# Kernel tuning notes

Hardware: AMD Instinct MI355X
Metric: run time of the kernel (lower is better)

## Reference

```python
import jax, jax.numpy as jnp
import numpy as np

KH, KW = 3, 3
STRIDE = (1, 1)
PAD = (1, 1)
DIL = (1, 1)
DG = 1  # num_deformable_groups


def _out_size(h, pad, dil, k, stride):
    return (h + 2 * pad - (dil * (k - 1) + 1)) // stride + 1


def setup_inputs() -> dict:
    key = jax.random.key(0)
    k1, k2, k3 = jax.random.split(key, 3)
    B, Cin, H, W = 8, 128, 64, 64
    Cout = 128
    Ho = _out_size(H, PAD[0], DIL[0], KH, STRIDE[0])
    Wo = _out_size(W, PAD[1], DIL[1], KW, STRIDE[1])
    x = jax.random.normal(k1, (B, Cin, H, W), jnp.float32)
    offset = jax.random.normal(k2, (B, 2 * DG * KH * KW, Ho, Wo), jnp.float32)
    n = Cin * KH * KW
    stdv = 1.0 / np.sqrt(n)
    weight = jax.random.uniform(k3, (Cout, Cin, KH, KW), jnp.float32, -stdv, stdv)
    return {"x": x, "offset": offset, "weight": weight}


def deform_conv2d(x, offset, weight):
    B, Cin, H, W = x.shape
    Cout, _, kh, kw = weight.shape
    K = kh * kw
    Ho = _out_size(H, PAD[0], DIL[0], kh, STRIDE[0])
    Wo = _out_size(W, PAD[1], DIL[1], kw, STRIDE[1])
    G = DG
    Cg = Cin // G

    # base sampling grid per kernel tap: [kh,kw,Ho,Wo]
    by = (jnp.arange(kh) * DIL[0])[:, None, None, None] + (jnp.arange(Ho) * STRIDE[0] - PAD[0])[None, None, :, None]
    bx = (jnp.arange(kw) * DIL[1])[None, :, None, None] + (jnp.arange(Wo) * STRIDE[1] - PAD[1])[None, None, None, :]
    by = jnp.broadcast_to(by, (kh, kw, Ho, Wo)).reshape(K, Ho, Wo).astype(x.dtype)
    bx = jnp.broadcast_to(bx, (kh, kw, Ho, Wo)).reshape(K, Ho, Wo).astype(x.dtype)

    # offset layout: channel = g*2*K + 2*k + {0: dy, 1: dx}
    off = offset.reshape(B, G, K, 2, Ho, Wo)
    py = by[None, None] + off[:, :, :, 0]  # [B,G,K,Ho,Wo]
    px = bx[None, None] + off[:, :, :, 1]

    y0 = jnp.floor(py).astype(jnp.int32)
    x0 = jnp.floor(px).astype(jnp.int32)
    wy = (py - y0).reshape(B, G, 1, -1)  # fractional parts, [B,G,1,K*Ho*Wo]
    wx = (px - x0).reshape(B, G, 1, -1)

    xg = x.reshape(B, G, Cg, H * W)
    N = K * Ho * Wo

    def gather(yi, xi):
        valid = ((yi >= 0) & (yi < H) & (xi >= 0) & (xi < W)).reshape(B, G, 1, N)
        idx = (jnp.clip(yi, 0, H - 1) * W + jnp.clip(xi, 0, W - 1)).reshape(B, G, 1, N)
        v = jnp.take_along_axis(xg, jnp.broadcast_to(idx, (B, G, Cg, N)), axis=3)
        return v * valid.astype(x.dtype)

    v00 = gather(y0, x0)
    v01 = gather(y0, x0 + 1)
    v10 = gather(y0 + 1, x0)
    v11 = gather(y0 + 1, x0 + 1)

    cols = (v00 * (1 - wy) * (1 - wx) + v01 * (1 - wy) * wx
            + v10 * wy * (1 - wx) + v11 * wy * wx)
    cols = cols.reshape(B, G, Cg, K, Ho, Wo)  # deformable im2col columns

    wr = weight.reshape(Cout, G, Cg, K)
    return jnp.einsum('ogck,bgcknm->bonm', wr, cols)


def reference(x, offset, weight):
    return deform_conv2d(x, offset, weight)
```

## Files before the change

### kernel.cpp

```cpp
#include <hip/hip_runtime.h>
#include <hip/hip_bf16.h>

typedef __attribute__((ext_vector_type(4))) float f32x4;
typedef __attribute__((ext_vector_type(2))) float f32x2;
typedef __attribute__((ext_vector_type(8))) short s16x8;
typedef __attribute__((ext_vector_type(4))) unsigned int u32x4;

__device__ __forceinline__ unsigned int f2bf(float f) {
  unsigned int u = __float_as_uint(f);
  u += 0x7fffu + ((u >> 16) & 1u);
  return u >> 16;
}
__device__ __forceinline__ f32x2 unpk(unsigned int p) {
  f32x2 r;
  r.x = __uint_as_float(p << 16);
  r.y = __uint_as_float(p & 0xffff0000u);
  return r;
}
__device__ __forceinline__ unsigned int pk_bf16(f32x2 s) {
  __hip_bfloat162 h = __float22bfloat162_rn(make_float2(s.x, s.y));
  unsigned int u;
  __builtin_memcpy(&u, &h, 4);
  return u;
}

__global__ __launch_bounds__(256) void xtrans_kernel(const float* __restrict__ x,
                                                     unsigned short* __restrict__ xt) {
  int t = blockIdx.x * 256 + threadIdx.x;
  int p  = t & 4095;
  int cg = (t >> 12) & 15;
  int b  = t >> 16;
  const float* xp = x + (((size_t)(b * 128 + cg * 8)) << 12) + p;
  unsigned int r[8];
#pragma unroll
  for (int j = 0; j < 8; ++j) r[j] = f2bf(xp[(size_t)j << 12]);
  u32x4 pk;
  pk.x = r[0] | (r[1] << 16);
  pk.y = r[2] | (r[3] << 16);
  pk.z = r[4] | (r[5] << 16);
  pk.w = r[6] | (r[7] << 16);
  *reinterpret_cast<u32x4*>(xt + ((((size_t)b << 12) + p) << 7) + cg * 8) = pk;
}

__global__ __launch_bounds__(256) void wtrans_kernel(const float* __restrict__ w,
                                                     unsigned short* __restrict__ wf) {
  int tid = blockIdx.x * 256 + threadIdx.x;
  int l  = tid & 63;
  int mt = (tid >> 6) & 7;
  int ch = tid >> 9;
  int cc = ch / 9, tap = ch - cc * 9;
  int co = mt * 16 + (l & 15);
  int cb = cc * 32 + (l >> 4) * 8;
  unsigned int r[8];
#pragma unroll
  for (int j = 0; j < 8; ++j)
    r[j] = f2bf(w[(co * 128 + cb + j) * 9 + tap]);
  u32x4 pk;
  pk.x = r[0] | (r[1] << 16);
  pk.y = r[2] | (r[3] << 16);
  pk.z = r[4] | (r[5] << 16);
  pk.w = r[6] | (r[7] << 16);
  *reinterpret_cast<u32x4*>(wf + (size_t)tid * 8) = pk;
}

__global__ __launch_bounds__(512, 1) void deform_kernel(const unsigned short* __restrict__ xt,
                                                        const float* __restrict__ off,
                                                        const unsigned short* __restrict__ wf,
                                                        float* __restrict__ out) {
  __shared__ __align__(16) unsigned char sWin[8 * 17408];
  __shared__ int    sPos[1152];
  __shared__ float4 sWt[1152];

  const int tid = threadIdx.x;
  const int bid = blockIdx.x;
  const int b   = bid & 7;
  const int ho0 = (bid >> 3) * 2;
  const int r0  = min(max(ho0 - 3, 0), 56);

  for (int r = tid; r < 1152; r += 512) {
    int row = (r >= 576) ? 1 : 0;
    int rr  = r - row * 576;
    int tap = rr >> 6, wo = rr & 63;
    int ho = ho0 + row;
    float dy = off[((b * 18 + 2 * tap)     * 64 + ho) * 64 + wo];
    float dx = off[((b * 18 + 2 * tap + 1) * 64 + ho) * 64 + wo];
    float py = (float)(ho + (tap / 3) - 1) + dy;
    float px = (float)(wo + (tap % 3) - 1) + dx;
    float fy = floorf(py), fx = floorf(px);
    int y0 = (int)fy, x0 = (int)fx;
    float wy = py - fy, wx = px - fx;
    float wt = (y0 >= 0 && y0 < 64) ? (1.f - wy) : 0.f;
    float wb = (y0 + 1 >= 0 && y0 + 1 < 64) ? wy : 0.f;
    int y0c = min(max(y0, 0), 63), y1c = min(max(y0 + 1, 0), 63);
    int bx; float wl, wr;
    if (x0 >= 0 && x0 <= 62)      { bx = x0; wl = 1.f - wx; wr = wx;       }
    else if (x0 == -1)            { bx = 0;  wl = wx;       wr = 0.f;      }
    else if (x0 == 63)            { bx = 62; wl = 0.f;      wr = 1.f - wx; }
    else                          { bx = 0;  wl = 0.f;      wr = 0.f;      }
    sPos[r] = (y0c * 64 + bx) | ((y1c != y0c) ? (1 << 15) : 0);
    sWt[r]  = make_float4(wt * wl, wt * wr, wb * wl, wb * wr);
  }

  {
    const unsigned short* xrow = xt + ((size_t)b << 19) + ((size_t)r0 << 13);
#pragma unroll
    for (int it = 0; it < 16; ++it) {
      int idx = it * 512 + tid;
      int c = idx & 15;
      int p = (idx >> 4) & 63;
      int r = idx >> 10;
      u32x4 v;
      __builtin_memcpy(&v, xrow + (((size_t)(r * 64 + p)) << 7) + c * 8, 16);
      *reinterpret_cast<u32x4*>(&sWin[r * 17408 + p * 272 + c * 16]) = v;
    }
  }
  __syncthreads();

  const int l  = tid & 63;
  const int w  = tid >> 6;
  const int ks = w & 3;
  const int mh = w >> 2;
  const int ln = l & 15;
  const int kg = l >> 4;
  const int koff = ks * 64 + kg * 16;

  const unsigned short* xtb = xt + ((size_t)b << 19) + ks * 32 + kg * 8;
  const unsigned short* wfb = wf + (size_t)l * 8;

  f32x4 acc[2][4][4] = {};

  for (int tap = 0; tap < 9; ++tap) {
    const int ch = ks * 9 + tap;

    s16x8 A[4];
    const unsigned short* wp = wfb + (size_t)(ch * 8 + mh * 4) * 512;
#pragma unroll
    for (int mt = 0; mt < 4; ++mt)
      A[mt] = *reinterpret_cast<const s16x8*>(wp + (size_t)mt * 512);

#pragma unroll
    for (int row = 0; row < 2; ++row) {
#pragma unroll
      for (int pg = 0; pg < 4; ++pg) {
        const int e = row * 576 + tap * 64 + pg * 16 + ln;
        const int    pp = sPos[e];
        const float4 wv = sWt[e];

        const int aX = pp & 4095;
        const int aY = aX + ((pp >> 9) & 64);
        const int tx  = aX & 63;
        const int twr = (aX >> 6) - r0;
        const int bwr = (aY >> 6) - r0;
        const bool tin = (unsigned)twr < 8u;
        const bool bin = (unsigned)bwr < 8u;

        u32x4 T0, T1, B0, B1;
        {
          int laT = (tin ? twr : 0) * 17408 + tx * 272 + koff;
          __builtin_memcpy(&T0, &sWin[laT],       16);
          __builtin_memcpy(&T1, &sWin[laT + 272], 16);
          int laB = (bin ? bwr : 0) * 17408 + tx * 272 + koff;
          __builtin_memcpy(&B0, &sWin[laB],       16);
          __builtin_memcpy(&B1, &sWin[laB + 272], 16);
        }
        if (!tin) {
          const unsigned short* p0 = xtb + ((size_t)aX << 7);
          __builtin_memcpy(&T0, p0,       16);
          __builtin_memcpy(&T1, p0 + 128, 16);
        }
        if (!bin) {
          const unsigned short* p1 = xtb + ((size_t)aY << 7);
          __builtin_memcpy(&B0, p1,       16);
          __builtin_memcpy(&B1, p1 + 128, 16);
        }

        u32x4 pk;
#pragma unroll
        for (int d = 0; d < 4; ++d) {
          f32x2 s = wv.x * unpk(T0[d]) + wv.y * unpk(T1[d])
                  + wv.z * unpk(B0[d]) + wv.w * unpk(B1[d]);
          pk[d] = pk_bf16(s);
        }
        s16x8 bfrag;
        __builtin_memcpy(&bfrag, &pk, 16);

#pragma unroll
        for (int mt = 0; mt < 4; ++mt)
          acc[row][pg][mt] = __builtin_amdgcn_mfma_f32_16x16x32_bf16(A[mt], bfrag,
                                                                     acc[row][pg][mt], 0, 0, 0);
      }
    }
  }

  float* sRed = reinterpret_cast<float*>(sWin);
#define WR_LDS                                                                 \
  { _Pragma("unroll") for (int row = 0; row < 2; ++row)                        \
    _Pragma("unroll") for (int pg = 0; pg < 4; ++pg)                           \
    _Pragma("unroll") for (int mt = 0; mt < 4; ++mt)                           \
      *reinterpret_cast<f32x4*>(&sRed[row * 8448 + (pg * 16 + ln) * 132 + mh * 64 + mt * 16 + kg * 4]) = acc[row][pg][mt]; }
#define RD_LDS                                                                 \
  { _Pragma("unroll") for (int row = 0; row < 2; ++row)                        \
    _Pragma("unroll") for (int pg = 0; pg < 4; ++pg)                           \
    _Pragma("unroll") for (int mt = 0; mt < 4; ++mt) {                         \
      f32x4 v = *reinterpret_cast<const f32x4*>(&sRed[row * 8448 + (pg * 16 + ln) * 132 + mh * 64 + mt * 16 + kg * 4]); \
      acc[row][pg][mt] += v; } }

  __syncthreads();
  if (ks == 1) WR_LDS
  __syncthreads();
  if (ks == 0) RD_LDS
  __syncthreads();
  if (ks == 3) WR_LDS
  __syncthreads();
  if (ks == 2) RD_LDS
  __syncthreads();
  if (ks == 2) WR_LDS
  __syncthreads();
  if (ks == 0) {
    RD_LDS
#pragma unroll
    for (int row = 0; row < 2; ++row)
#pragma unroll
      for (int pg = 0; pg < 4; ++pg)
#pragma unroll
        for (int mt = 0; mt < 4; ++mt)
#pragma unroll
          for (int rg = 0; rg < 4; ++rg) {
            int co = mh * 64 + mt * 16 + kg * 4 + rg;
            out[((b * 128 + co) * 64 + ho0 + row) * 64 + pg * 16 + ln] = acc[row][pg][mt][rg];
          }
  }
#undef WR_LDS
#undef RD_LDS
}

extern "C" void kernel_launch(void* const* d_in, const int* in_sizes, int n_in,
                              void* d_out, int out_size, void* d_ws, size_t ws_size,
                              hipStream_t stream) {
  (void)in_sizes; (void)n_in; (void)out_size; (void)ws_size;
  const float* x   = (const float*)d_in[0];
  const float* off = (const float*)d_in[1];
  const float* w   = (const float*)d_in[2];
  float* out = (float*)d_out;
  unsigned short* xt = (unsigned short*)d_ws;
  unsigned short* wf = (unsigned short*)d_ws + (8388608 / 2);

  xtrans_kernel<<<2048, 256, 0, stream>>>(x, xt);
  wtrans_kernel<<<72, 256, 0, stream>>>(w, wf);
  deform_kernel<<<256, 512, 0, stream>>>(xt, off, wf, out);
}
```

Before: 120.0 us.

## Assign one output row per wave-pair and stage output through LDS for vector stores

Changes the warp work split so that each wave handles one output row and all 128 output channels, replacing the earlier split of two rows by 64 channels. Each bilinear-interpolated B fragment is now reused across 8 MFMAs instead of 4, so the gather and interpolation work per row is no longer duplicated across the two channel halves. The final output is staged through LDS so it can be written as float4 stores instead of scalar strided stores. The cost is more accumulator registers (32 f32x4) and 8 A fragments per wave, which raises register pressure and may lower occupancy.

```diff
diff --git a/kernel.cpp b/kernel.cpp
--- a/kernel.cpp
+++ b/kernel.cpp
@@ -116,94 +116,90 @@
   }
   __syncthreads();
 
-  const int l  = tid & 63;
-  const int w  = tid >> 6;
-  const int ks = w & 3;
-  const int mh = w >> 2;
-  const int ln = l & 15;
-  const int kg = l >> 4;
+  const int l   = tid & 63;
+  const int w   = tid >> 6;
+  const int ks  = w & 3;
+  const int row = w >> 2;
+  const int ln  = l & 15;
+  const int kg  = l >> 4;
   const int koff = ks * 64 + kg * 16;
+  const int ho  = ho0 + row;
 
   const unsigned short* xtb = xt + ((size_t)b << 19) + ks * 32 + kg * 8;
   const unsigned short* wfb = wf + (size_t)l * 8;
 
-  f32x4 acc[2][4][4] = {};
+  f32x4 acc[4][8] = {};
 
   for (int tap = 0; tap < 9; ++tap) {
     const int ch = ks * 9 + tap;
 
-    s16x8 A[4];
-    const unsigned short* wp = wfb + (size_t)(ch * 8 + mh * 4) * 512;
-#pragma unroll
-    for (int mt = 0; mt < 4; ++mt)
+    s16x8 A[8];
+    const unsigned short* wp = wfb + (size_t)(ch * 8) * 512;
+#pragma unroll
+    for (int mt = 0; mt < 8; ++mt)
       A[mt] = *reinterpret_cast<const s16x8*>(wp + (size_t)mt * 512);
 
 #pragma unroll
-    for (int row = 0; row < 2; ++row) {
-#pragma unroll
-      for (int pg = 0; pg < 4; ++pg) {
-        const int e = row * 576 + tap * 64 + pg * 16 + ln;
-        const int    pp = sPos[e];
-        const float4 wv = sWt[e];
-
-        const int aX = pp & 4095;
-        const int aY = aX + ((pp >> 9) & 64);
-        const int tx  = aX & 63;
-        const int twr = (aX >> 6) - r0;
-        const int bwr = (aY >> 6) - r0;
-        const bool tin = (unsigned)twr < 8u;
-        const bool bin = (unsigned)bwr < 8u;
-
-        u32x4 T0, T1, B0, B1;
-        {
-          int laT = (tin ? twr : 0) * 17408 + tx * 272 + koff;
-          __builtin_memcpy(&T0, &sWin[laT],       16);
-          __builtin_memcpy(&T1, &sWin[laT + 272], 16);
-          int laB = (bin ? bwr : 0) * 17408 + tx * 272 + koff;
-          __builtin_memcpy(&B0, &sWin[laB],       16);
-          __builtin_memcpy(&B1, &sWin[laB + 272], 16);
-        }
-        if (!tin) {
-          const unsigned short* p0 = xtb + ((size_t)aX << 7);
-          __builtin_memcpy(&T0, p0,       16);
-          __builtin_memcpy(&T1, p0 + 128, 16);
-        }
-        if (!bin) {
-          const unsigned short* p1 = xtb + ((size_t)aY << 7);
-          __builtin_memcpy(&B0, p1,       16);
-          __builtin_memcpy(&B1, p1 + 128, 16);
-        }
-
-        u32x4 pk;
-#pragma unroll
-        for (int d = 0; d < 4; ++d) {
-          f32x2 s = wv.x * unpk(T0[d]) + wv.y * unpk(T1[d])
-                  + wv.z * unpk(B0[d]) + wv.w * unpk(B1[d]);
-          pk[d] = pk_bf16(s);
-        }
-        s16x8 bfrag;
-        __builtin_memcpy(&bfrag, &pk, 16);
-
-#pragma unroll
-        for (int mt = 0; mt < 4; ++mt)
-          acc[row][pg][mt] = __builtin_amdgcn_mfma_f32_16x16x32_bf16(A[mt], bfrag,
-                                                                     acc[row][pg][mt], 0, 0, 0);
-      }
-    }
-  }
-
-  float* sRed = reinterpret_cast<float*>(sWin);
+    for (int pg = 0; pg < 4; ++pg) {
+      const int e = row * 576 + tap * 64 + pg * 16 + ln;
+      const int    pp = sPos[e];
+      const float4 wv = sWt[e];
+
+      const int aX = pp & 4095;
+      const int aY = aX + ((pp >> 9) & 64);
+      const int tx  = aX & 63;
+      const int twr = (aX >> 6) - r0;
+      const int bwr = (aY >> 6) - r0;
+      const bool tin = (unsigned)twr < 8u;
+      const bool bin = (unsigned)bwr < 8u;
+
+      u32x4 T0, T1, B0, B1;
+      {
+        int laT = (tin ? twr : 0) * 17408 + tx * 272 + koff;
+        __builtin_memcpy(&T0, &sWin[laT],       16);
+        __builtin_memcpy(&T1, &sWin[laT + 272], 16);
+        int laB = (bin ? bwr : 0) * 17408 + tx * 272 + koff;
+        __builtin_memcpy(&B0, &sWin[laB],       16);
+        __builtin_memcpy(&B1, &sWin[laB + 272], 16);
+      }
+      if (!tin) {
+        const unsigned short* p0 = xtb + ((size_t)aX << 7);
+        __builtin_memcpy(&T0, p0,       16);
+        __builtin_memcpy(&T1, p0 + 128, 16);
+      }
+      if (!bin) {
+        const unsigned short* p1 = xtb + ((size_t)aY << 7);
+        __builtin_memcpy(&B0, p1,       16);
+        __builtin_memcpy(&B1, p1 + 128, 16);
+      }
+
+      u32x4 pk;
+#pragma unroll
+      for (int d = 0; d < 4; ++d) {
+        f32x2 s = wv.x * unpk(T0[d]) + wv.y * unpk(T1[d])
+                + wv.z * unpk(B0[d]) + wv.w * unpk(B1[d]);
+        pk[d] = pk_bf16(s);
+      }
+      s16x8 bfrag;
+      __builtin_memcpy(&bfrag, &pk, 16);
+
+#pragma unroll
+      for (int mt = 0; mt < 8; ++mt)
+        acc[pg][mt] = __builtin_amdgcn_mfma_f32_16x16x32_bf16(A[mt], bfrag,
+                                                              acc[pg][mt], 0, 0, 0);
+    }
+  }
+
+  float* sF = reinterpret_cast<float*>(sWin);
 #define WR_LDS                                                                 \
-  { _Pragma("unroll") for (int row = 0; row < 2; ++row)                        \
-    _Pragma("unroll") for (int pg = 0; pg < 4; ++pg)                           \
-    _Pragma("unroll") for (int mt = 0; mt < 4; ++mt)                           \
-      *reinterpret_cast<f32x4*>(&sRed[row * 8448 + (pg * 16 + ln) * 132 + mh * 64 + mt * 16 + kg * 4]) = acc[row][pg][mt]; }
+  { _Pragma("unroll") for (int pg = 0; pg < 4; ++pg)                           \
+    _Pragma("unroll") for (int mt = 0; mt < 8; ++mt)                           \
+      *reinterpret_cast<f32x4*>(&sF[row * 8448 + (pg * 16 + ln) * 132 + mt * 16 + kg * 4]) = acc[pg][mt]; }
 #define RD_LDS                                                                 \
-  { _Pragma("unroll") for (int row = 0; row < 2; ++row)                        \
-    _Pragma("unroll") for (int pg = 0; pg < 4; ++pg)                           \
-    _Pragma("unroll") for (int mt = 0; mt < 4; ++mt) {                         \
-      f32x4 v = *reinterpret_cast<const f32x4*>(&sRed[row * 8448 + (pg * 16 + ln) * 132 + mh * 64 + mt * 16 + kg * 4]); \
-      acc[row][pg][mt] += v; } }
+  { _Pragma("unroll") for (int pg = 0; pg < 4; ++pg)                           \
+    _Pragma("unroll") for (int mt = 0; mt < 8; ++mt) {                         \
+      f32x4 v = *reinterpret_cast<const f32x4*>(&sF[row * 8448 + (pg * 16 + ln) * 132 + mt * 16 + kg * 4]); \
+      acc[pg][mt] += v; } }
 
   __syncthreads();
   if (ks == 1) WR_LDS
@@ -216,22 +212,34 @@
   __syncthreads();
   if (ks == 2) WR_LDS
   __syncthreads();
-  if (ks == 0) {
-    RD_LDS
-#pragma unroll
-    for (int row = 0; row < 2; ++row)
-#pragma unroll
-      for (int pg = 0; pg < 4; ++pg)
-#pragma unroll
-        for (int mt = 0; mt < 4; ++mt)
-#pragma unroll
-          for (int rg = 0; rg < 4; ++rg) {
-            int co = mh * 64 + mt * 16 + kg * 4 + rg;
-            out[((b * 128 + co) * 64 + ho0 + row) * 64 + pg * 16 + ln] = acc[row][pg][mt][rg];
-          }
-  }
+  if (ks == 0) RD_LDS
 #undef WR_LDS
 #undef RD_LDS
+
+  {
+    const int b2 = 16896 + row * 8704;
+    if (ks == 0) {
+#pragma unroll
+      for (int pg = 0; pg < 4; ++pg)
+#pragma unroll
+        for (int mt = 0; mt < 8; ++mt)
+#pragma unroll
+          for (int rg = 0; rg < 4; ++rg)
+            sF[b2 + (mt * 16 + kg * 4 + rg) * 68 + pg * 16 + ln] = acc[pg][mt][rg];
+    }
+    __syncthreads();
+    if (ks == 0) {
+      const int q4  = l & 15;
+      const int ch2 = l >> 4;
+      float* ob = out + (((size_t)b * 128) * 64 + ho) * 64 + q4 * 4;
+#pragma unroll
+      for (int i = 0; i < 32; ++i) {
+        int co = ch2 * 32 + i;
+        f32x4 v = *reinterpret_cast<const f32x4*>(&sF[b2 + co * 68 + q4 * 4]);
+        *reinterpret_cast<f32x4*>(ob + (size_t)co * 4096) = v;
+      }
+    }
+  }
 }
 
 extern "C" void kernel_launch(void* const* d_in, const int* in_sizes, int n_in,
```

New measurement: 108.0 us. 1.11x faster.
